# Optimization experiments

Measured on AMD Instinct MI355X. Metric: run time of the kernel, lower is better.

## Reference

```python
import jax, jax.numpy as jnp
import numpy as np


def setup_inputs() -> dict:
    key = jax.random.key(0)
    x = jax.random.normal(key, (16, 64, 224, 224), dtype=jnp.float32)
    return {"x": x}


def reference(x):
    # FLC pooling: FFT2 (norm='forward'), center-crop low frequencies, inverse FFT2.
    # Note: torch.fft.fftshift with default dims shifts ALL axes, but since the
    # crop only touches the last two axes, the shifts on batch/channel axes are
    # exactly undone by the subsequent ifftshift; shifting only (-2,-1) is
    # mathematically identical.
    H, W = x.shape[2], x.shape[3]
    Xf = jnp.fft.fftshift(jnp.fft.fft2(x, norm='forward'), axes=(-2, -1))
    low = Xf[:, :, H // 4: (H // 4) * 3, W // 4: (W // 4) * 3]
    out = jnp.fft.ifft2(jnp.fft.ifftshift(low, axes=(-2, -1)), norm='forward').real
    return out
```

## Files before the change

kernel.cpp:

```cpp
#include <hip/hip_runtime.h>
#include <math.h>

#define HH 224
#define WW 224
#define OH 112
#define OW 112
#define NCH 1024
#define YP 232

typedef __attribute__((ext_vector_type(8))) short s16x8;
typedef __attribute__((ext_vector_type(4))) float f32x4;

static __device__ __host__ __forceinline__ unsigned short f2bf(float f) {
    union { float f; unsigned int u; } v; v.f = f;
    unsigned int r = (v.u + 0x7FFFu + ((v.u >> 16) & 1u)) >> 16;
    return (unsigned short)r;
}

__global__ void lr_init_kernel(unsigned short* __restrict__ lrbf) {
    int idx = blockIdx.x * blockDim.x + threadIdx.x;
    if (idx >= OH * HH) return;
    int p = idx / HH;
    int m = idx % HH;
    float val = 0.0f;
    if ((m & 1) == 0) {
        val = (m == 2 * p) ? 0.5f : 0.0f;
    } else {
        int j = m >> 1;
        int r = 2 * p - m;
        float a = (float)M_PI * (float)r * (1.0f / 224.0f);
        float sg = ((p - j) & 1) ? 1.0f : -1.0f;
        val = sg * (cosf(a) / sinf(a)) * (1.0f / 224.0f);
    }
    lrbf[p * HH + m] = f2bf(val);
}

__launch_bounds__(448, 2)
__global__ void flc_mfma_kernel(const float* __restrict__ x,
                                const unsigned short* __restrict__ lrbf,
                                float* __restrict__ out) {
    __shared__ float x_s[32 * WW];
    __shared__ unsigned short y_s[OH * YP];
    __shared__ float wsum[7];

    const int c = blockIdx.x;
    const int t = threadIdx.x;
    const int w = t >> 6;
    const int l = t & 63;
    const int lr16 = l & 15;
    const int g = l >> 4;

    const float* __restrict__ xc = x + (size_t)c * (HH * WW);

    f32x4 accA[7][2];
    #pragma unroll
    for (int i = 0; i < 7; ++i) {
        accA[i][0] = f32x4{0.f, 0.f, 0.f, 0.f};
        accA[i][1] = f32x4{0.f, 0.f, 0.f, 0.f};
    }
    float spart = 0.0f;

    for (int ks = 0; ks < 7; ++ks) {
        const int k0 = ks * 32;
        __syncthreads();
        #pragma unroll
        for (int i = 0; i < 4; ++i) {
            const float* gp = xc + k0 * WW + (i * 448 + t) * 4;
            char* lp = (char*)x_s + (size_t)(i * 448 + t) * 16;
            __builtin_amdgcn_global_load_lds(
                (const __attribute__((address_space(1))) unsigned int*)gp,
                (__attribute__((address_space(3))) unsigned int*)lp, 16, 0, 0);
        }
        __syncthreads();

        s16x8 af[7];
        #pragma unroll
        for (int pt = 0; pt < 7; ++pt) {
            int row = pt * 16 + lr16;
            af[pt] = *(const s16x8*)(lrbf + row * HH + k0 + 8 * g);
        }
        #pragma unroll
        for (int nt = 0; nt < 2; ++nt) {
            const int col = 32 * w + 16 * nt + lr16;
            s16x8 bv;
            #pragma unroll
            for (int j = 0; j < 8; ++j)
                bv[j] = (short)f2bf(x_s[(8 * g + j) * WW + col]);
            #pragma unroll
            for (int pt = 0; pt < 7; ++pt)
                accA[pt][nt] = __builtin_amdgcn_mfma_f32_16x16x32_bf16(
                    af[pt], bv, accA[pt][nt], 0, 0, 0);
        }
        #pragma unroll
        for (int i = 0; i < 4; ++i) {
            int e = t + 448 * i;
            int jj = e / 112, kk = e % 112;
            float v = x_s[(2 * jj + 1) * WW + (2 * kk + 1)];
            spart += ((jj + kk) & 1) ? -v : v;
        }
    }

    #pragma unroll
    for (int off = 32; off > 0; off >>= 1)
        spart += __shfl_down(spart, off, 64);
    if (l == 0) wsum[w] = spart;

    #pragma unroll
    for (int pt = 0; pt < 7; ++pt) {
        #pragma unroll
        for (int nt = 0; nt < 2; ++nt) {
            const int col = 32 * w + 16 * nt + lr16;
            #pragma unroll
            for (int r = 0; r < 4; ++r) {
                int row = pt * 16 + 4 * g + r;
                y_s[row * YP + col] = f2bf(accA[pt][nt][r]);
            }
        }
    }
    __syncthreads();

    f32x4 accB[7];
    #pragma unroll
    for (int i = 0; i < 7; ++i) accB[i] = f32x4{0.f, 0.f, 0.f, 0.f};

    for (int ks = 0; ks < 7; ++ks) {
        const int k0 = ks * 32;
        const int q = 16 * w + lr16;
        s16x8 bf = *(const s16x8*)(lrbf + q * HH + k0 + 8 * g);
        #pragma unroll
        for (int pt = 0; pt < 7; ++pt) {
            int row = pt * 16 + lr16;
            s16x8 yf = *(const s16x8*)(&y_s[row * YP + k0 + 8 * g]);
            accB[pt] = __builtin_amdgcn_mfma_f32_16x16x32_bf16(yf, bf, accB[pt], 0, 0, 0);
        }
    }

    float ssum = 0.0f;
    #pragma unroll
    for (int i = 0; i < 7; ++i) ssum += wsum[i];
    const float s = ssum * (1.0f / (224.0f * 224.0f));

    float* __restrict__ oc = out + (size_t)c * (OH * OW);
    const int q = 16 * w + lr16;
    #pragma unroll
    for (int pt = 0; pt < 7; ++pt) {
        #pragma unroll
        for (int r = 0; r < 4; ++r) {
            int p = pt * 16 + 4 * g + r;
            oc[p * OW + q] = accB[pt][r] - (((p + q) & 1) ? -s : s);
        }
    }
}

extern "C" void kernel_launch(void* const* d_in, const int* in_sizes, int n_in,
                              void* d_out, int out_size, void* d_ws, size_t ws_size,
                              hipStream_t stream) {
    const float* x = (const float*)d_in[0];
    float* out = (float*)d_out;
    unsigned short* lrbf = (unsigned short*)d_ws;

    hipLaunchKernelGGL(lr_init_kernel, dim3((OH * HH + 255) / 256), dim3(256), 0, stream, lrbf);
    hipLaunchKernelGGL(flc_mfma_kernel, dim3(NCH), dim3(448), 0, stream, x, lrbf, out);
}
```

Before: 311.8 us.

## Double-buffer input tiles and widen block to 896 threads with tile-distributed second GEMM

Each block now has 896 threads (14 waves) and double-buffers the 32-row input slabs in LDS, so the next slab's global-to-LDS load is issued before the MFMA work on the current slab. That leaves one barrier per step instead of two. Each wave computes one 16-column tile in the first GEMM. The second GEMM is split into 49 16x16 output tiles spread round-robin across the 14 waves. LDS use roughly doubles for the x buffer and occupancy drops to one block per CU, so latency hiding now depends on the in-block prefetch.

```diff
diff --git a/kernel.cpp b/kernel.cpp
--- a/kernel.cpp
+++ b/kernel.cpp
@@ -7,6 +7,8 @@
 #define OW 112
 #define NCH 1024
 #define YP 232
+#define NT 896
+#define SR 32
 
 typedef __attribute__((ext_vector_type(8))) short s16x8;
 typedef __attribute__((ext_vector_type(4))) float f32x4;
@@ -35,13 +37,13 @@
     lrbf[p * HH + m] = f2bf(val);
 }
 
-__launch_bounds__(448, 2)
+__launch_bounds__(896, 1)
 __global__ void flc_mfma_kernel(const float* __restrict__ x,
                                 const unsigned short* __restrict__ lrbf,
                                 float* __restrict__ out) {
-    __shared__ float x_s[32 * WW];
+    __shared__ float x_s[2][SR * WW];
     __shared__ unsigned short y_s[OH * YP];
-    __shared__ float wsum[7];
+    __shared__ float wsum[14];
 
     const int c = blockIdx.x;
     const int t = threadIdx.x;
@@ -52,52 +54,64 @@
 
     const float* __restrict__ xc = x + (size_t)c * (HH * WW);
 
-    f32x4 accA[7][2];
-    #pragma unroll
-    for (int i = 0; i < 7; ++i) {
-        accA[i][0] = f32x4{0.f, 0.f, 0.f, 0.f};
-        accA[i][1] = f32x4{0.f, 0.f, 0.f, 0.f};
-    }
-    float spart = 0.0f;
-
-    for (int ks = 0; ks < 7; ++ks) {
-        const int k0 = ks * 32;
-        __syncthreads();
+    {
         #pragma unroll
-        for (int i = 0; i < 4; ++i) {
-            const float* gp = xc + k0 * WW + (i * 448 + t) * 4;
-            char* lp = (char*)x_s + (size_t)(i * 448 + t) * 16;
+        for (int k2 = 0; k2 < 2; ++k2) {
+            const float* g2 = xc + (k2 * NT + t) * 4;
+            char* lp = (char*)(&x_s[0][0]) + (size_t)(k2 * NT + t) * 16;
             __builtin_amdgcn_global_load_lds(
-                (const __attribute__((address_space(1))) unsigned int*)gp,
+                (const __attribute__((address_space(1))) unsigned int*)g2,
                 (__attribute__((address_space(3))) unsigned int*)lp, 16, 0, 0);
         }
-        __syncthreads();
+    }
+    __syncthreads();
+
+    f32x4 accA[7];
+    #pragma unroll
+    for (int i = 0; i < 7; ++i) accA[i] = f32x4{0.f, 0.f, 0.f, 0.f};
+    float spart = 0.0f;
+    const int col = (w << 4) + lr16;
+
+    for (int i = 0; i < 7; ++i) {
+        const int cur = i & 1;
+        const int k0 = i * SR;
+        const float* __restrict__ xs = &x_s[cur][0];
 
         s16x8 af[7];
         #pragma unroll
-        for (int pt = 0; pt < 7; ++pt) {
-            int row = pt * 16 + lr16;
-            af[pt] = *(const s16x8*)(lrbf + row * HH + k0 + 8 * g);
+        for (int pt = 0; pt < 7; ++pt)
+            af[pt] = *(const s16x8*)(lrbf + (pt * 16 + lr16) * HH + k0 + 8 * g);
+
+        if (i < 6) {
+            const float* gp = xc + (k0 + SR) * WW;
+            char* xdst = (char*)(&x_s[cur ^ 1][0]);
+            #pragma unroll
+            for (int k2 = 0; k2 < 2; ++k2) {
+                const float* g2 = gp + (k2 * NT + t) * 4;
+                char* lp = xdst + (size_t)(k2 * NT + t) * 16;
+                __builtin_amdgcn_global_load_lds(
+                    (const __attribute__((address_space(1))) unsigned int*)g2,
+                    (__attribute__((address_space(3))) unsigned int*)lp, 16, 0, 0);
+            }
         }
+
+        s16x8 bv;
         #pragma unroll
-        for (int nt = 0; nt < 2; ++nt) {
-            const int col = 32 * w + 16 * nt + lr16;
-            s16x8 bv;
-            #pragma unroll
-            for (int j = 0; j < 8; ++j)
-                bv[j] = (short)f2bf(x_s[(8 * g + j) * WW + col]);
-            #pragma unroll
-            for (int pt = 0; pt < 7; ++pt)
-                accA[pt][nt] = __builtin_amdgcn_mfma_f32_16x16x32_bf16(
-                    af[pt], bv, accA[pt][nt], 0, 0, 0);
-        }
+        for (int j = 0; j < 8; ++j)
+            bv[j] = (short)f2bf(xs[(8 * g + j) * WW + col]);
         #pragma unroll
-        for (int i = 0; i < 4; ++i) {
-            int e = t + 448 * i;
+        for (int pt = 0; pt < 7; ++pt)
+            accA[pt] = __builtin_amdgcn_mfma_f32_16x16x32_bf16(af[pt], bv, accA[pt], 0, 0, 0);
+
+        #pragma unroll
+        for (int rr = 0; rr < 2; ++rr) {
+            int e = t + NT * rr;
             int jj = e / 112, kk = e % 112;
-            float v = x_s[(2 * jj + 1) * WW + (2 * kk + 1)];
+            float v = xs[(2 * jj + 1) * WW + (2 * kk + 1)];
             spart += ((jj + kk) & 1) ? -v : v;
         }
+
+        __syncthreads();
     }
 
     #pragma unroll
@@ -108,46 +122,31 @@
     #pragma unroll
     for (int pt = 0; pt < 7; ++pt) {
         #pragma unroll
-        for (int nt = 0; nt < 2; ++nt) {
-            const int col = 32 * w + 16 * nt + lr16;
-            #pragma unroll
-            for (int r = 0; r < 4; ++r) {
-                int row = pt * 16 + 4 * g + r;
-                y_s[row * YP + col] = f2bf(accA[pt][nt][r]);
-            }
-        }
+        for (int r = 0; r < 4; ++r)
+            y_s[(pt * 16 + 4 * g + r) * YP + col] = f2bf(accA[pt][r]);
     }
     __syncthreads();
 
-    f32x4 accB[7];
-    #pragma unroll
-    for (int i = 0; i < 7; ++i) accB[i] = f32x4{0.f, 0.f, 0.f, 0.f};
-
-    for (int ks = 0; ks < 7; ++ks) {
-        const int k0 = ks * 32;
-        const int q = 16 * w + lr16;
-        s16x8 bf = *(const s16x8*)(lrbf + q * HH + k0 + 8 * g);
-        #pragma unroll
-        for (int pt = 0; pt < 7; ++pt) {
-            int row = pt * 16 + lr16;
-            s16x8 yf = *(const s16x8*)(&y_s[row * YP + k0 + 8 * g]);
-            accB[pt] = __builtin_amdgcn_mfma_f32_16x16x32_bf16(yf, bf, accB[pt], 0, 0, 0);
-        }
-    }
-
     float ssum = 0.0f;
     #pragma unroll
-    for (int i = 0; i < 7; ++i) ssum += wsum[i];
+    for (int w2 = 0; w2 < 14; ++w2) ssum += wsum[w2];
     const float s = ssum * (1.0f / (224.0f * 224.0f));
 
     float* __restrict__ oc = out + (size_t)c * (OH * OW);
-    const int q = 16 * w + lr16;
-    #pragma unroll
-    for (int pt = 0; pt < 7; ++pt) {
+    for (int T = w; T < 49; T += 14) {
+        const int pi = T / 7, qi = T % 7;
+        f32x4 acc = f32x4{0.f, 0.f, 0.f, 0.f};
+        #pragma unroll
+        for (int ks = 0; ks < 7; ++ks) {
+            s16x8 ya = *(const s16x8*)(&y_s[(pi * 16 + lr16) * YP + ks * 32 + 8 * g]);
+            s16x8 bq = *(const s16x8*)(lrbf + (qi * 16 + lr16) * HH + ks * 32 + 8 * g);
+            acc = __builtin_amdgcn_mfma_f32_16x16x32_bf16(ya, bq, acc, 0, 0, 0);
+        }
+        const int q = qi * 16 + lr16;
         #pragma unroll
         for (int r = 0; r < 4; ++r) {
-            int p = pt * 16 + 4 * g + r;
-            oc[p * OW + q] = accB[pt][r] - (((p + q) & 1) ? -s : s);
+            int p = pi * 16 + 4 * g + r;
+            oc[p * OW + q] = acc[r] - (((p + q) & 1) ? -s : s);
         }
     }
 }
@@ -160,5 +159,5 @@
     unsigned short* lrbf = (unsigned short*)d_ws;
 
     hipLaunchKernelGGL(lr_init_kernel, dim3((OH * HH + 255) / 256), dim3(256), 0, stream, lrbf);
-    hipLaunchKernelGGL(flc_mfma_kernel, dim3(NCH), dim3(448), 0, stream, x, lrbf, out);
+    hipLaunchKernelGGL(flc_mfma_kernel, dim3(NCH), dim3(NT), 0, stream, x, lrbf, out);
 }
```

After: 334.8 us. 7.4% more time.
